# Optimization experiments

Hardware: AMD Instinct MI355X
Metric: run time of the kernel (lower is better)

## Reference

```python
import jax, jax.numpy as jnp
import numpy as np

B, N1, N2, D, H, L, ITERS = 256, 64, 64, 256, 8, 18, 200
DH = D // H
LAYER_NAMES = ['self', 'cross'] * 9
OFFSET_MULT, NORMAL_MULT = 0.5, 10.0
FLIP = np.array([1.0, -1.0, -1.0], dtype=np.float32)


def setup_inputs() -> dict:
    key = jax.random.key(0)
    ks = jax.random.split(key, 16)
    s = 0.02
    inp = {
        'planeApp1': jax.random.normal(ks[0], (B, N1, D), jnp.float32),
        'planeApp2': jax.random.normal(ks[1], (B, N2, D), jnp.float32),
        'matcher_inputCam': jax.random.normal(ks[2], (B, 7), jnp.float32),
        'parameters1_local': jax.random.normal(ks[3], (B, N1, 3), jnp.float32),
        'parameters2_local': jax.random.normal(ks[4], (B, N2, 3), jnp.float32),
        'app_W': jax.random.normal(ks[5], (D, D), jnp.float32) * s,
        'app_b': jnp.zeros((D,), jnp.float32),
        'desc_W': jax.random.normal(ks[6], (D, D), jnp.float32) * s,
        'desc_b': jnp.zeros((D,), jnp.float32),
        'bin_score': jnp.asarray(1.0, jnp.float32),
        'gnn_Wq': jax.random.normal(ks[7], (L, D, D), jnp.float32) * s,
        'gnn_Wk': jax.random.normal(ks[8], (L, D, D), jnp.float32) * s,
        'gnn_Wv': jax.random.normal(ks[9], (L, D, D), jnp.float32) * s,
        'gnn_Wm': jax.random.normal(ks[10], (L, D, D), jnp.float32) * s,
        'gnn_W1': jax.random.normal(ks[11], (L, 2 * D, 2 * D), jnp.float32) * s,
        'gnn_W2': jax.random.normal(ks[12], (L, 2 * D, D), jnp.float32) * s,
        'gnn_ln1_g': jnp.ones((L, D), jnp.float32),
        'gnn_ln1_b': jnp.zeros((L, D), jnp.float32),
        'gnn_ln2_g': jnp.ones((L, D), jnp.float32),
        'gnn_ln2_b': jnp.zeros((L, D), jnp.float32),
    }
    return inp


def _layer_norm(x, g, b):
    m = jnp.mean(x, -1, keepdims=True)
    v = jnp.var(x, -1, keepdims=True)
    return (x - m) * jax.lax.rsqrt(v + 1e-5) * g + b


def _normalize(x):
    return x / jnp.clip(jnp.linalg.norm(x, axis=-1, keepdims=True), 1e-12)


def _quat_to_rot(q):
    q = q / jnp.linalg.norm(q, axis=-1, keepdims=True)
    w, x, y, z = q[:, 0], q[:, 1], q[:, 2], q[:, 3]
    R = jnp.stack([1 - 2 * (y * y + z * z), 2 * (x * y - w * z), 2 * (x * z + w * y),
                   2 * (x * y + w * z), 1 - 2 * (x * x + z * z), 2 * (y * z - w * x),
                   2 * (x * z - w * y), 2 * (y * z + w * x), 1 - 2 * (x * x + y * y)], axis=-1)
    return R.reshape(-1, 3, 3)


def _warp(plane, quat, tran):
    # plane [B,n,3], quat [B,4], tran [B,3] -> warped plane params [B,n,3]
    R = _quat_to_rot(quat)
    end = jnp.einsum('bij,bnj->bni', R, plane * FLIP) + tran[:, None, :]
    b = end - tran[:, None, :]
    scale = jnp.sum(end * b, -1) / (jnp.linalg.norm(b, axis=-1) + 1e-5) ** 2
    return scale[..., None] * b


def _lin_attn(q, k, v):
    # LoFTR linear attention; q [B,N,H,DH], k/v [B,M,H,DH]
    Q = jax.nn.elu(q) + 1.0
    K = jax.nn.elu(k) + 1.0
    v_len = v.shape[1]
    KV = jnp.einsum('bmhd,bmhe->bhde', K, v / v_len)
    Zden = 1.0 / (jnp.einsum('bnhd,bhd->bnh', Q, K.sum(1)) + 1e-6)
    return jnp.einsum('bnhd,bhde,bnh->bnhe', Q, KV, Zden) * v_len


def _enc_layer(x, src, Wq, Wk, Wv, Wm, W1, W2, g1, be1, g2, be2):
    Bx, N, _ = x.shape
    M = src.shape[1]
    q = (x @ Wq).reshape(Bx, N, H, DH)
    k = (src @ Wk).reshape(Bx, M, H, DH)
    v = (src @ Wv).reshape(Bx, M, H, DH)
    msg = _lin_attn(q, k, v).reshape(Bx, N, D)
    msg = _layer_norm(msg @ Wm, g1, be1)
    msg = _layer_norm(jax.nn.relu(jnp.concatenate([x, msg], -1) @ W1) @ W2, g2, be2)
    return x + msg


def reference(planeApp1, planeApp2, matcher_inputCam, parameters1_local, parameters2_local,
              app_W, app_b, desc_W, desc_b, bin_score,
              gnn_Wq, gnn_Wk, gnn_Wv, gnn_Wm, gnn_W1, gnn_W2,
              gnn_ln1_g, gnn_ln1_b, gnn_ln2_g, gnn_ln2_b):
    tran, quat = matcher_inputCam[:, :3], matcher_inputCam[:, 3:]
    # --- geometric priors (detached in the original) ---
    p2w = parameters2_local * FLIP  # warp with pose_n=1, no rot/tran
    offset2 = jnp.linalg.norm(p2w, axis=-1)  # [B,N2]
    normal2 = _normalize(p2w)
    p1_r = _warp(parameters1_local, quat, tran * 0.0)
    normal1_r = _normalize(p1_r)
    normal_dist = jnp.arccos(jnp.clip(jnp.einsum('bnd,bmd->bnm', normal1_r, normal2), -1.0, 1.0)) / np.pi * 180.0
    p1_rt = _warp(parameters1_local, quat, tran)
    offset1 = jnp.linalg.norm(p1_rt, axis=-1)  # [B,N1]
    normal1_rt = _normalize(p1_rt)
    nTn_rt = jnp.einsum('bnd,bmd->bnm', normal1_rt, normal2)
    od = jnp.where(nTn_rt < 0,
                   jnp.abs(offset1[:, :, None] + offset2[:, None, :]),
                   jnp.abs(offset1[:, :, None] - offset2[:, None, :]))
    offset_dist = jax.lax.stop_gradient(jnp.clip(od, 1e-10, 5.0))
    normal_dist = jax.lax.stop_gradient(normal_dist)
    # --- appearance projection (1x1 Conv1d == per-token linear) ---
    x0 = planeApp1 @ app_W + app_b
    x1 = planeApp2 @ app_W + app_b
    for i, name in enumerate(LAYER_NAMES):
        p = (gnn_Wq[i], gnn_Wk[i], gnn_Wv[i], gnn_Wm[i], gnn_W1[i], gnn_W2[i],
             gnn_ln1_g[i], gnn_ln1_b[i], gnn_ln2_g[i], gnn_ln2_b[i])
        if name == 'self':
            x0, x1 = _enc_layer(x0, x0, *p), _enc_layer(x1, x1, *p)
        else:
            x0, x1 = _enc_layer(x0, x1, *p), _enc_layer(x1, x0, *p)
    d1 = x0 @ desc_W + desc_b
    d2 = x1 @ desc_W + desc_b
    scores = jnp.einsum('bnd,bmd->bnm', d1, d2) / jnp.sqrt(jnp.float32(D))
    scores = scores - offset_dist / OFFSET_MULT - normal_dist / NORMAL_MULT
    # --- padded optimal transport (all rows/cols valid -> no -inf masking) ---
    pc = jnp.broadcast_to(bin_score, (B, N1, 1))
    pr = jnp.broadcast_to(bin_score, (B, 1, N2 + 1))
    Z = jnp.concatenate([jnp.concatenate([scores, pc], axis=2), pr], axis=1)  # [B,N1+1,N2+1]
    norm = -jnp.log(jnp.float32(N1 + N2))
    log_mu = jnp.broadcast_to(jnp.concatenate([jnp.full((N1,), norm), (jnp.log(jnp.float32(N2)) + norm)[None]]), (B, N1 + 1))
    log_nu = jnp.broadcast_to(jnp.concatenate([jnp.full((N2,), norm), (jnp.log(jnp.float32(N1)) + norm)[None]]), (B, N2 + 1))

    def step(carry, _):
        u, v = carry
        u = log_mu - jax.nn.logsumexp(Z + v[:, None, :], axis=2)
        v = log_nu - jax.nn.logsumexp(Z + u[:, :, None], axis=1)
        return (u, v), None

    (u, v), _ = jax.lax.scan(step, (jnp.zeros_like(log_mu), jnp.zeros_like(log_nu)), None, length=ITERS)
    return Z + u[:, :, None] + v[:, None, :] - norm
```

## Files before the change

kernel.cpp:

```cpp
#include <hip/hip_runtime.h>
#include <math.h>
#include <stddef.h>
#include <stdint.h>

typedef unsigned short u16;
typedef unsigned int   u32;

static constexpr int B_   = 256;
static constexpr int N_   = 64;
static constexpr int D_   = 256;
static constexpr int L_   = 18;
static constexpr int RM   = B_ * N_;
static constexpr int RM2  = 2 * RM;
static constexpr size_t SZb = (size_t)RM2 * D_;

typedef __attribute__((ext_vector_type(8))) short bf16x8;
typedef __attribute__((ext_vector_type(4))) float f32x4;

__device__ __forceinline__ float b2f(u16 u) {
    return __uint_as_float(((u32)u) << 16);
}
__device__ __forceinline__ u16 f2b(float f) {
    u32 x = __float_as_uint(f);
    return (u16)((x + 0x7FFFu + ((x >> 16) & 1u)) >> 16);
}
__device__ __forceinline__ void gl_lds16(const void* g, void* l) {
    __builtin_amdgcn_global_load_lds(
        (const __attribute__((address_space(1))) u32*)g,
        (__attribute__((address_space(3))) u32*)l, 16, 0, 0);
}

template<int CONCAT, int RELU, int BIAS, int OUTF, int OUTB>
__global__ __launch_bounds__(256)
void mgemm(const u16* __restrict__ A1, const u16* __restrict__ A2,
           const u16* __restrict__ Bt, const float* __restrict__ bias,
           float* __restrict__ Cf, u16* __restrict__ Cb,
           int M, int K, int splitn)
{
    __shared__ u16 As[128 * 64];
    __shared__ u16 Bs[128 * 64];
    const int tid  = threadIdx.x;
    const int w    = tid >> 6;
    const int lane = tid & 63;
    const int wr   = w >> 1, wc = w & 1;
    const int row0 = blockIdx.x * 128;
    const int col0 = blockIdx.y * 128;
    const int lr   = lane & 15;
    const int lk   = (lane >> 4) * 8;
    const int srow = lane >> 3;
    const int schk = (lane & 7) * 8;

    f32x4 acc[4][4];
    #pragma unroll
    for (int m = 0; m < 4; ++m)
        #pragma unroll
        for (int n = 0; n < 4; ++n)
            acc[m][n] = (f32x4){0.f, 0.f, 0.f, 0.f};

    for (int k0 = 0; k0 < K; k0 += 64) {
        const u16* Aeff; int kloc, lda;
        if (CONCAT) {
            if (k0 < 256) { Aeff = A1; kloc = k0; } else { Aeff = A2; kloc = k0 - 256; }
            lda = 256;
        } else { Aeff = A1; kloc = k0; lda = K; }
        #pragma unroll
        for (int q = 0; q < 4; ++q) {
            const int i = w * 4 + q;
            gl_lds16(Aeff + (size_t)(row0 + i * 8 + srow) * lda + kloc + schk,
                     &As[i * 512]);
            gl_lds16(Bt + (size_t)(col0 + i * 8 + srow) * K + k0 + schk,
                     &Bs[i * 512]);
        }
        __syncthreads();
        #pragma unroll
        for (int kk = 0; kk < 2; ++kk) {
            bf16x8 af[4], bfr[4];
            #pragma unroll
            for (int m = 0; m < 4; ++m)
                af[m] = *(const bf16x8*)&As[(wr * 64 + m * 16 + lr) * 64 + kk * 32 + lk];
            #pragma unroll
            for (int n = 0; n < 4; ++n)
                bfr[n] = *(const bf16x8*)&Bs[(wc * 64 + n * 16 + lr) * 64 + kk * 32 + lk];
            #pragma unroll
            for (int m = 0; m < 4; ++m)
                #pragma unroll
                for (int n = 0; n < 4; ++n)
                    acc[m][n] = __builtin_amdgcn_mfma_f32_16x16x32_bf16(
                        af[m], bfr[n], acc[m][n], 0, 0, 0);
        }
        __syncthreads();
    }

    const size_t cbase = (size_t)(col0 / splitn) * (size_t)M * splitn;
    const int lc0 = col0 % splitn;
    #pragma unroll
    for (int m = 0; m < 4; ++m) {
        #pragma unroll
        for (int n = 0; n < 4; ++n) {
            const int gc = lc0 + wc * 64 + n * 16 + (lane & 15);
            #pragma unroll
            for (int r = 0; r < 4; ++r) {
                const int gr = row0 + wr * 64 + m * 16 + (lane >> 4) * 4 + r;
                float v = acc[m][n][r];
                if (BIAS) v += bias[gc];
                if (RELU) v = fmaxf(v, 0.f);
                const size_t idx = cbase + (size_t)gr * splitn + gc;
                if (OUTF) Cf[idx] = v;
                if (OUTB) Cb[idx] = f2b(v);
            }
        }
    }
}

template<int RES>
__global__ __launch_bounds__(256)
void mgemm_ln(const u16* __restrict__ A, const u16* __restrict__ Bt,
              const float* __restrict__ g, const float* __restrict__ beta,
              float* __restrict__ resf, u16* __restrict__ outb, int K)
{
    __shared__ u16 As[64 * 64];
    __shared__ u16 Bs[256 * 64];
    __shared__ float rs[4][64], rq[4][64];
    const int tid  = threadIdx.x;
    const int w    = tid >> 6;
    const int lane = tid & 63;
    const int row0 = blockIdx.x * 64;
    const int lr   = lane & 15;
    const int lk   = (lane >> 4) * 8;
    const int srow = lane >> 3;
    const int schk = (lane & 7) * 8;

    f32x4 acc[4][4];
    #pragma unroll
    for (int m = 0; m < 4; ++m)
        #pragma unroll
        for (int n = 0; n < 4; ++n)
            acc[m][n] = (f32x4){0.f, 0.f, 0.f, 0.f};

    for (int k0 = 0; k0 < K; k0 += 64) {
        #pragma unroll
        for (int q = 0; q < 2; ++q) {
            const int i = w * 2 + q;
            gl_lds16(A + (size_t)(row0 + i * 8 + srow) * K + k0 + schk,
                     &As[i * 512]);
        }
        #pragma unroll
        for (int q = 0; q < 8; ++q) {
            const int i = w * 8 + q;
            gl_lds16(Bt + (size_t)(i * 8 + srow) * K + k0 + schk,
                     &Bs[i * 512]);
        }
        __syncthreads();
        #pragma unroll
        for (int kk = 0; kk < 2; ++kk) {
            bf16x8 af[4], bfr[4];
            #pragma unroll
            for (int m = 0; m < 4; ++m)
                af[m] = *(const bf16x8*)&As[(m * 16 + lr) * 64 + kk * 32 + lk];
            #pragma unroll
            for (int n = 0; n < 4; ++n)
                bfr[n] = *(const bf16x8*)&Bs[(w * 64 + n * 16 + lr) * 64 + kk * 32 + lk];
            #pragma unroll
            for (int m = 0; m < 4; ++m)
                #pragma unroll
                for (int n = 0; n < 4; ++n)
                    acc[m][n] = __builtin_amdgcn_mfma_f32_16x16x32_bf16(
                        af[m], bfr[n], acc[m][n], 0, 0, 0);
        }
        __syncthreads();
    }

    #pragma unroll
    for (int m = 0; m < 4; ++m) {
        #pragma unroll
        for (int r = 0; r < 4; ++r) {
            float s  = acc[m][0][r] + acc[m][1][r] + acc[m][2][r] + acc[m][3][r];
            float s2 = acc[m][0][r]*acc[m][0][r] + acc[m][1][r]*acc[m][1][r]
                     + acc[m][2][r]*acc[m][2][r] + acc[m][3][r]*acc[m][3][r];
            #pragma unroll
            for (int o = 1; o < 16; o <<= 1) {
                s  += __shfl_xor(s,  o);
                s2 += __shfl_xor(s2, o);
            }
            if ((lane & 15) == 0) {
                const int row = m * 16 + (lane >> 4) * 4 + r;
                rs[w][row] = s; rq[w][row] = s2;
            }
        }
    }
    __syncthreads();
    if (tid < 64) {
        const float s = rs[0][tid] + rs[1][tid] + rs[2][tid] + rs[3][tid];
        const float q = rq[0][tid] + rq[1][tid] + rq[2][tid] + rq[3][tid];
        const float mean = s * (1.f / 256.f);
        const float var  = q * (1.f / 256.f) - mean * mean;
        rs[0][tid] = mean;
        rq[0][tid] = rsqrtf(var + 1e-5f);
    }
    __syncthreads();

    float gc[4], bc[4];
    #pragma unroll
    for (int n = 0; n < 4; ++n) {
        const int col = w * 64 + n * 16 + lr;
        gc[n] = g[col]; bc[n] = beta[col];
    }
    #pragma unroll
    for (int m = 0; m < 4; ++m) {
        #pragma unroll
        for (int r = 0; r < 4; ++r) {
            const int row  = m * 16 + (lane >> 4) * 4 + r;
            const float mean = rs[0][row], inv = rq[0][row];
            const int gr = row0 + row;
            #pragma unroll
            for (int n = 0; n < 4; ++n) {
                const int col = w * 64 + n * 16 + lr;
                const size_t idx = (size_t)gr * 256 + col;
                float y = (acc[m][n][r] - mean) * inv * gc[n] + bc[n];
                if (RES) {
                    const float o = resf[idx] + y;
                    resf[idx] = o;
                    outb[idx] = f2b(o);
                } else {
                    outb[idx] = f2b(y);
                }
            }
        }
    }
}

__global__ __launch_bounds__(256)
void wtrans_kernel(const float* __restrict__ W, u16* __restrict__ Wt,
                   int K, int N, size_t in_lstride, size_t out_lstride,
                   int row_off, int ldk)
{
    __shared__ float T[64][65];
    const int k0 = blockIdx.x * 64, n0 = blockIdx.y * 64, l = blockIdx.z;
    const int t = threadIdx.x;
    const int r = t >> 2, c0 = (t & 3) * 16;
    const float* src = W + (size_t)l * in_lstride;
    #pragma unroll
    for (int q = 0; q < 4; ++q) {
        float4 v = *(const float4*)&src[(size_t)(k0 + r) * N + n0 + c0 + q * 4];
        T[r][c0 + q * 4 + 0] = v.x; T[r][c0 + q * 4 + 1] = v.y;
        T[r][c0 + q * 4 + 2] = v.z; T[r][c0 + q * 4 + 3] = v.w;
    }
    __syncthreads();
    u16 tmp[16];
    #pragma unroll
    for (int i = 0; i < 16; ++i) tmp[i] = f2b(T[c0 + i][r]);
    u16* dst = Wt + (size_t)l * out_lstride + (size_t)(row_off + n0 + r) * ldk + k0 + c0;
    *(uint4*)&dst[0] = *(const uint4*)&tmp[0];
    *(uint4*)&dst[8] = *(const uint4*)&tmp[8];
}

__global__ __launch_bounds__(256)
void cvt_kernel(const float* __restrict__ src, u16* __restrict__ dst, int n4)
{
    int i = blockIdx.x * 256 + threadIdx.x;
    if (i >= n4) return;
    float4 v = *(const float4*)&src[(size_t)i * 4];
    u16 o[4] = {f2b(v.x), f2b(v.y), f2b(v.z), f2b(v.w)};
    *(uint2*)&dst[(size_t)i * 4] = *(const uint2*)&o[0];
}

__global__ __launch_bounds__(256)
void attn_kernel(const u16* __restrict__ Q, const u16* __restrict__ K,
                 const u16* __restrict__ V, u16* __restrict__ Mout, int selfl)
{
    const int bid = blockIdx.x;
    const int h = bid & 7;
    const int b = (bid >> 3) & 255;
    const int s = bid >> 11;
    const int ss = selfl ? s : (1 - s);
    const size_t qoff = ((size_t)(s  * RM) + b * N_) * D_ + h * 32;
    const size_t koff = ((size_t)(ss * RM) + b * N_) * D_ + h * 32;

    __shared__ float Ks[64][32];
    __shared__ float Vs[64][32];
    __shared__ float Qs[64][33];
    __shared__ float KV[32][32];
    __shared__ float Ksum[32];
    __shared__ float zden[64];

    const int t = threadIdx.x;
    {
        const int m = t >> 2, d0 = (t & 3) * 8;
        uint4 kq = *(const uint4*)&K[koff + (size_t)m * D_ + d0];
        uint4 vq = *(const uint4*)&V[koff + (size_t)m * D_ + d0];
        uint4 qq = *(const uint4*)&Q[qoff + (size_t)m * D_ + d0];
        const u16* kp = (const u16*)&kq;
        const u16* vp = (const u16*)&vq;
        const u16* qp = (const u16*)&qq;
        #pragma unroll
        for (int j = 0; j < 8; ++j) {
            float kx = b2f(kp[j]);
            Ks[m][d0 + j] = kx > 0.f ? kx + 1.f : __expf(kx);
            Vs[m][d0 + j] = b2f(vp[j]);
            float qx = b2f(qp[j]);
            Qs[m][d0 + j] = qx > 0.f ? qx + 1.f : __expf(qx);
        }
    }
    __syncthreads();
    if (t < 32) {
        float sacc = 0.f;
        for (int m = 0; m < 64; ++m) sacc += Ks[m][t];
        Ksum[t] = sacc;
    }
    for (int i = t; i < 32 * 32; i += 256) {
        const int d = i >> 5, e = i & 31;
        float acc = 0.f;
        for (int m = 0; m < 64; ++m) acc += Ks[m][d] * Vs[m][e];
        KV[d][e] = acc * (1.f / 64.f);
    }
    __syncthreads();
    if (t < 64) {
        float acc = 0.f;
        for (int d = 0; d < 32; ++d) acc += Qs[t][d] * Ksum[d];
        zden[t] = 1.f / (acc + 1e-6f);
    }
    __syncthreads();
    const int n = t >> 2, eg = t & 3;
    float acc[8] = {0.f,0.f,0.f,0.f,0.f,0.f,0.f,0.f};
    for (int d = 0; d < 32; ++d) {
        const float qv = Qs[n][d];
        #pragma unroll
        for (int j = 0; j < 8; ++j) acc[j] += qv * KV[d][eg * 8 + j];
    }
    const float zm = zden[n] * 64.f;
    u16 o[8];
    #pragma unroll
    for (int j = 0; j < 8; ++j) o[j] = f2b(acc[j] * zm);
    *(uint4*)&Mout[qoff + (size_t)n * D_ + eg * 8] = *(const uint4*)&o[0];
}

__global__ __launch_bounds__(64)
void geom_kernel(const float* __restrict__ cam, const float* __restrict__ p1,
                 const float* __restrict__ p2, float* __restrict__ pen)
{
    const int b = blockIdx.x;
    const int n = threadIdx.x;

    const float tx = cam[b*7+0], ty = cam[b*7+1], tz = cam[b*7+2];
    float qw = cam[b*7+3], qx = cam[b*7+4], qy = cam[b*7+5], qz = cam[b*7+6];
    const float qn = rsqrtf(qw*qw + qx*qx + qy*qy + qz*qz);
    qw *= qn; qx *= qn; qy *= qn; qz *= qn;
    const float r00 = 1.f - 2.f*(qy*qy + qz*qz), r01 = 2.f*(qx*qy - qw*qz), r02 = 2.f*(qx*qz + qw*qy);
    const float r10 = 2.f*(qx*qy + qw*qz), r11 = 1.f - 2.f*(qx*qx + qz*qz), r12 = 2.f*(qy*qz - qw*qx);
    const float r20 = 2.f*(qx*qz - qw*qy), r21 = 2.f*(qy*qz + qw*qx), r22 = 1.f - 2.f*(qx*qx + qy*qy);

    const float px =  p1[((size_t)b*64 + n)*3 + 0];
    const float py = -p1[((size_t)b*64 + n)*3 + 1];
    const float pz = -p1[((size_t)b*64 + n)*3 + 2];
    const float ex = r00*px + r01*py + r02*pz;
    const float ey = r10*px + r11*py + r12*pz;
    const float ez = r20*px + r21*py + r22*pz;
    const float el2 = ex*ex + ey*ey + ez*ez;
    const float el  = sqrtf(el2);
    float den = el + 1e-5f; den = den * den;
    const float sr  = el2 / den;
    const float prx = sr*ex, pry = sr*ey, prz = sr*ez;
    const float prl = fmaxf(sqrtf(prx*prx + pry*pry + prz*prz), 1e-12f);
    const float n1rx = prx/prl, n1ry = pry/prl, n1rz = prz/prl;
    const float dot_eb = (ex+tx)*ex + (ey+ty)*ey + (ez+tz)*ez;
    const float st  = dot_eb / den;
    const float ptx = st*ex, pty = st*ey, ptz = st*ez;
    const float o1  = sqrtf(ptx*ptx + pty*pty + ptz*ptz);
    const float ptl = fmaxf(o1, 1e-12f);
    const float n1tx = ptx/ptl, n1ty = pty/ptl, n1tz = ptz/ptl;
    const float ux =  p2[((size_t)b*64 + n)*3 + 0];
    const float uy = -p2[((size_t)b*64 + n)*3 + 1];
    const float uz = -p2[((size_t)b*64 + n)*3 + 2];
    const float o2 = sqrtf(ux*ux + uy*uy + uz*uz);
    const float ul = fmaxf(o2, 1e-12f);

    __shared__ float S[64][4];
    S[n][0] = ux/ul; S[n][1] = uy/ul; S[n][2] = uz/ul; S[n][3] = o2;
    __syncthreads();

    const float RAD2DEG = 57.295779513082323f;
    for (int m = 0; m < 64; ++m) {
        const float nx = S[m][0], ny = S[m][1], nz = S[m][2], o2m = S[m][3];
        float cosr = n1rx*nx + n1ry*ny + n1rz*nz;
        cosr = fminf(fmaxf(cosr, -1.f), 1.f);
        const float ndist = acosf(cosr) * RAD2DEG;
        const float cost = n1tx*nx + n1ty*ny + n1tz*nz;
        float od = (cost < 0.f) ? fabsf(o1 + o2m) : fabsf(o1 - o2m);
        od = fminf(fmaxf(od, 1e-10f), 5.f);
        pen[((size_t)b*64 + n)*64 + m] = od * 2.f + ndist * 0.1f;
    }
}

__global__ __launch_bounds__(256)
void zbuild_kernel(const float* __restrict__ dfeat, const float* __restrict__ pen,
                   const float* __restrict__ binp, float* __restrict__ Z)
{
    const int b = blockIdx.x;
    const float* d1 = dfeat + (size_t)(b * 64) * 256;
    const float* d2 = dfeat + (size_t)(RM + b * 64) * 256;
    __shared__ float D1[64][65], D2[64][65];
    const int tid = threadIdx.x;
    const int txx = tid & 15, tyy = tid >> 4;
    float acc[4][4] = {{0.f,0.f,0.f,0.f},{0.f,0.f,0.f,0.f},
                       {0.f,0.f,0.f,0.f},{0.f,0.f,0.f,0.f}};
    for (int c0 = 0; c0 < 256; c0 += 64) {
        __syncthreads();
        for (int i = tid; i < 64 * 64; i += 256) {
            const int r = i >> 6, c = i & 63;
            D1[r][c] = d1[(size_t)r * 256 + c0 + c];
            D2[r][c] = d2[(size_t)r * 256 + c0 + c];
        }
        __syncthreads();
        for (int c = 0; c < 64; ++c) {
            const float a0 = D1[tyy*4+0][c], a1 = D1[tyy*4+1][c];
            const float a2 = D1[tyy*4+2][c], a3 = D1[tyy*4+3][c];
            const float b0 = D2[txx*4+0][c], b1 = D2[txx*4+1][c];
            const float b2 = D2[txx*4+2][c], b3 = D2[txx*4+3][c];
            acc[0][0] += a0*b0; acc[0][1] += a0*b1; acc[0][2] += a0*b2; acc[0][3] += a0*b3;
            acc[1][0] += a1*b0; acc[1][1] += a1*b1; acc[1][2] += a1*b2; acc[1][3] += a1*b3;
            acc[2][0] += a2*b0; acc[2][1] += a2*b1; acc[2][2] += a2*b2; acc[2][3] += a2*b3;
            acc[3][0] += a3*b0; acc[3][1] += a3*b1; acc[3][2] += a3*b2; acc[3][3] += a3*b3;
        }
    }
    const float bin = *binp;
    #pragma unroll
    for (int i = 0; i < 4; ++i)
        #pragma unroll
        for (int j = 0; j < 4; ++j) {
            const int n = tyy*4 + i, m = txx*4 + j;
            Z[(size_t)b*4225 + n*65 + m] =
                acc[i][j] * (1.f/16.f) - pen[((size_t)b*64 + n)*64 + m];
        }
    if (tid < 65) Z[(size_t)b*4225 + 64*65 + tid] = bin;
    if (tid < 64) Z[(size_t)b*4225 + tid*65 + 64] = bin;
}

__global__ __launch_bounds__(576)
void sinkhorn_kernel(const float* __restrict__ Zin, float* __restrict__ out)
{
    const int b = blockIdx.x;
    __shared__ float uu[65], vv[65];
    const int t  = threadIdx.x;
    const int rr = t >> 3, l8 = t & 7;
    const int act = (rr < 65);
    const float LOG2E = 1.4426950408889634f;
    const float LN2   = 0.69314718055994531f;

    float zrow[9], zcol[9];
    #pragma unroll
    for (int p = 0; p < 9; ++p) {
        const int j = l8 + p * 8;
        const int ok = act && (j < 65);
        zrow[p] = ok ? Zin[(size_t)b * 4225 + rr * 65 + j] * LOG2E : -3.0e38f;
        zcol[p] = ok ? Zin[(size_t)b * 4225 + j * 65 + rr] * LOG2E : -3.0e38f;
    }
    if (t < 65) vv[t] = 0.f;
    __syncthreads();

    const float mu2 = (rr < 64) ? -7.0f : -1.0f;

    for (int it = 0; it < 200; ++it) {
        {
            float m = -3.0e38f, sum = 0.f, vals[9];
            #pragma unroll
            for (int p = 0; p < 9; ++p) {
                const int j = l8 + p * 8;
                vals[p] = zrow[p] + vv[j < 65 ? j : 0];
                m = fmaxf(m, vals[p]);
            }
            #pragma unroll
            for (int p = 0; p < 9; ++p) sum += exp2f(vals[p] - m);
            #pragma unroll
            for (int o = 1; o < 8; o <<= 1) {
                const float om = __shfl_xor(m, o);
                const float os = __shfl_xor(sum, o);
                const float nm = fmaxf(m, om);
                sum = sum * exp2f(m - nm) + os * exp2f(om - nm);
                m = nm;
            }
            if (act && l8 == 0) uu[rr] = mu2 - (m + log2f(sum));
        }
        __syncthreads();
        {
            float m = -3.0e38f, sum = 0.f, vals[9];
            #pragma unroll
            for (int p = 0; p < 9; ++p) {
                const int j = l8 + p * 8;
                vals[p] = zcol[p] + uu[j < 65 ? j : 0];
                m = fmaxf(m, vals[p]);
            }
            #pragma unroll
            for (int p = 0; p < 9; ++p) sum += exp2f(vals[p] - m);
            #pragma unroll
            for (int o = 1; o < 8; o <<= 1) {
                const float om = __shfl_xor(m, o);
                const float os = __shfl_xor(sum, o);
                const float nm = fmaxf(m, om);
                sum = sum * exp2f(m - nm) + os * exp2f(om - nm);
                m = nm;
            }
            if (act && l8 == 0) vv[rr] = mu2 - (m + log2f(sum));
        }
        __syncthreads();
    }
    if (act) {
        const float ur = uu[rr];
        #pragma unroll
        for (int p = 0; p < 9; ++p) {
            const int j = l8 + p * 8;
            if (j < 65)
                out[(size_t)b * 4225 + rr * 65 + j] =
                    (zrow[p] + ur + vv[j] + 7.0f) * LN2;
        }
    }
}

extern "C" void kernel_launch(void* const* d_in, const int* in_sizes, int n_in,
                              void* d_out, int out_size, void* d_ws, size_t ws_size,
                              hipStream_t stream)
{
    const float* planeApp1 = (const float*)d_in[0];
    const float* planeApp2 = (const float*)d_in[1];
    const float* cam       = (const float*)d_in[2];
    const float* p1        = (const float*)d_in[3];
    const float* p2        = (const float*)d_in[4];
    const float* app_W     = (const float*)d_in[5];
    const float* app_b     = (const float*)d_in[6];
    const float* desc_W    = (const float*)d_in[7];
    const float* desc_b    = (const float*)d_in[8];
    const float* bin_score = (const float*)d_in[9];
    const float* Wq        = (const float*)d_in[10];
    const float* Wk        = (const float*)d_in[11];
    const float* Wv        = (const float*)d_in[12];
    const float* Wm        = (const float*)d_in[13];
    const float* W1        = (const float*)d_in[14];
    const float* W2        = (const float*)d_in[15];
    const float* ln1g      = (const float*)d_in[16];
    const float* ln1b      = (const float*)d_in[17];
    const float* ln2g      = (const float*)d_in[18];
    const float* ln2b      = (const float*)d_in[19];

    const size_t wq_elems   = (size_t)L_ * 768 * 256;
    const size_t wm_elems   = (size_t)L_ * 256 * 256;
    const size_t w1_elems   = (size_t)L_ * 512 * 512;
    const size_t w2_elems   = (size_t)L_ * 256 * 512;
    const size_t need = 5 * SZb * 2 + SZb * 4 + (size_t)B_ * 4096 * 4 +
        (wq_elems + wm_elems + w1_elems + w2_elems + 2 * 65536) * 2;
    if (ws_size < need) return;

    u16* Xb = (u16*)d_ws;
    u16* Qb = Xb + SZb;
    u16* Kb = Qb + SZb;
    u16* Vb = Kb + SZb;
    u16* Tb = Vb + SZb;
    float* Xf  = (float*)(Tb + SZb);
    float* pen = Xf + SZb;
    u16* wqkv = (u16*)(pen + (size_t)B_ * 4096);
    u16* wmt  = wqkv + wq_elems;
    u16* w1t  = wmt + wm_elems;
    u16* w2t  = w1t + w1_elems;
    u16* appt = w2t + w2_elems;
    u16* dsct = appt + 65536;
    float* outp = (float*)d_out;

    wtrans_kernel<<<dim3(4, 4, L_), 256, 0, stream>>>(Wq, wqkv, 256, 256, 65536, 768*256, 0,   256);
    wtrans_kernel<<<dim3(4, 4, L_), 256, 0, stream>>>(Wk, wqkv, 256, 256, 65536, 768*256, 256, 256);
    wtrans_kernel<<<dim3(4, 4, L_), 256, 0, stream>>>(Wv, wqkv, 256, 256, 65536, 768*256, 512, 256);
    wtrans_kernel<<<dim3(4, 4, L_), 256, 0, stream>>>(Wm, wmt,  256, 256, 65536, 65536,   0,   256);
    wtrans_kernel<<<dim3(8, 8, L_), 256, 0, stream>>>(W1, w1t,  512, 512, 262144, 262144, 0,   512);
    wtrans_kernel<<<dim3(8, 4, L_), 256, 0, stream>>>(W2, w2t,  512, 256, 131072, 131072, 0,   512);
    wtrans_kernel<<<dim3(4, 4, 1),  256, 0, stream>>>(app_W,  appt, 256, 256, 65536, 65536, 0, 256);
    wtrans_kernel<<<dim3(4, 4, 1),  256, 0, stream>>>(desc_W, dsct, 256, 256, 65536, 65536, 0, 256);

    cvt_kernel<<<(RM * D_ / 4 + 255) / 256, 256, 0, stream>>>(planeApp1, Qb, RM * D_ / 4);
    cvt_kernel<<<(RM * D_ / 4 + 255) / 256, 256, 0, stream>>>(planeApp2, Qb + (size_t)RM * D_, RM * D_ / 4);

    geom_kernel<<<B_, 64, 0, stream>>>(cam, p1, p2, pen);

    mgemm<0,0,1,1,1><<<dim3(RM2/128, 2), 256, 0, stream>>>(
        Qb, nullptr, appt, app_b, Xf, Xb, RM2, 256, 256);

    for (int i = 0; i < L_; ++i) {
        const int selfl = (i % 2 == 0) ? 1 : 0;
        mgemm<0,0,0,0,1><<<dim3(RM2/128, 6), 256, 0, stream>>>(
            Xb, nullptr, wqkv + (size_t)i*768*256, nullptr, nullptr, Qb, RM2, 256, 256);
        attn_kernel<<<2 * B_ * 8, 256, 0, stream>>>(Qb, Kb, Vb, Qb, selfl);
        mgemm_ln<0><<<RM2/64, 256, 0, stream>>>(
            Qb, wmt + (size_t)i*65536, ln1g + i*256, ln1b + i*256,
            nullptr, Tb, 256);
        mgemm<1,1,0,0,1><<<dim3(RM2/128, 4), 256, 0, stream>>>(
            Xb, Tb, w1t + (size_t)i*262144, nullptr, nullptr, Qb, RM2, 512, 512);
        mgemm_ln<1><<<RM2/64, 256, 0, stream>>>(
            Qb, w2t + (size_t)i*131072, ln2g + i*256, ln2b + i*256,
            Xf, Xb, 512);
    }

    mgemm<0,0,1,1,0><<<dim3(RM2/128, 2), 256, 0, stream>>>(
        Xb, nullptr, dsct, desc_b, (float*)Qb, nullptr, RM2, 256, 256);

    zbuild_kernel<<<B_, 256, 0, stream>>>((float*)Qb, pen, bin_score, (float*)Vb);
    sinkhorn_kernel<<<B_, 576, 0, stream>>>((float*)Vb, outp);
}
```

Baseline: 3.336 ms.

## Double-buffer GEMM LDS tiles, enlarge LN-GEMM tile, simplify Sinkhorn reductions

Both GEMM kernels now prefetch the next K-slice into a second LDS buffer while the current one feeds the MFMAs, with K a compile-time constant so the loop fully unrolls. The fused GEMM+LayerNorm kernel moves to 128-row tiles on 512 threads, halving how often each block reloads the full 256-column weight slab. The Sinkhorn loop replaces its online max/sum shuffle merge with a max reduction followed by a plain sum reduction, and pads the u/v arrays so index clamping is no longer needed. The cost is more LDS per block (about 100KB for the LN kernel), which lowers occupancy.

```diff
diff --git a/kernel.cpp b/kernel.cpp
--- a/kernel.cpp
+++ b/kernel.cpp
@@ -30,15 +30,16 @@
         (__attribute__((address_space(3))) u32*)l, 16, 0, 0);
 }
 
-template<int CONCAT, int RELU, int BIAS, int OUTF, int OUTB>
+template<int K, int CONCAT, int RELU, int BIAS, int OUTF, int OUTB>
 __global__ __launch_bounds__(256)
 void mgemm(const u16* __restrict__ A1, const u16* __restrict__ A2,
            const u16* __restrict__ Bt, const float* __restrict__ bias,
            float* __restrict__ Cf, u16* __restrict__ Cb,
-           int M, int K, int splitn)
-{
-    __shared__ u16 As[128 * 64];
-    __shared__ u16 Bs[128 * 64];
+           int M, int splitn)
+{
+    constexpr int NT = K / 64;
+    __shared__ u16 As[2][128 * 64];
+    __shared__ u16 Bs[2][128 * 64];
     const int tid  = threadIdx.x;
     const int w    = tid >> 6;
     const int lane = tid & 63;
@@ -50,14 +51,8 @@
     const int srow = lane >> 3;
     const int schk = (lane & 7) * 8;
 
-    f32x4 acc[4][4];
-    #pragma unroll
-    for (int m = 0; m < 4; ++m)
-        #pragma unroll
-        for (int n = 0; n < 4; ++n)
-            acc[m][n] = (f32x4){0.f, 0.f, 0.f, 0.f};
-
-    for (int k0 = 0; k0 < K; k0 += 64) {
+    auto stage = [&](int t, int buf) {
+        const int k0 = t * 64;
         const u16* Aeff; int kloc, lda;
         if (CONCAT) {
             if (k0 < 256) { Aeff = A1; kloc = k0; } else { Aeff = A2; kloc = k0 - 256; }
@@ -67,20 +62,34 @@
         for (int q = 0; q < 4; ++q) {
             const int i = w * 4 + q;
             gl_lds16(Aeff + (size_t)(row0 + i * 8 + srow) * lda + kloc + schk,
-                     &As[i * 512]);
-            gl_lds16(Bt + (size_t)(col0 + i * 8 + srow) * K + k0 + schk,
-                     &Bs[i * 512]);
-        }
-        __syncthreads();
+                     &As[buf][i * 512]);
+            gl_lds16(Bt + (size_t)(col0 + i * 8 + srow) * K + t * 64 + schk,
+                     &Bs[buf][i * 512]);
+        }
+    };
+
+    f32x4 acc[4][4];
+    #pragma unroll
+    for (int m = 0; m < 4; ++m)
+        #pragma unroll
+        for (int n = 0; n < 4; ++n)
+            acc[m][n] = (f32x4){0.f, 0.f, 0.f, 0.f};
+
+    stage(0, 0);
+    __syncthreads();
+    #pragma unroll
+    for (int t = 0; t < NT; ++t) {
+        const int cur = t & 1;
+        if (t + 1 < NT) stage(t + 1, cur ^ 1);
         #pragma unroll
         for (int kk = 0; kk < 2; ++kk) {
             bf16x8 af[4], bfr[4];
             #pragma unroll
             for (int m = 0; m < 4; ++m)
-                af[m] = *(const bf16x8*)&As[(wr * 64 + m * 16 + lr) * 64 + kk * 32 + lk];
+                af[m] = *(const bf16x8*)&As[cur][(wr * 64 + m * 16 + lr) * 64 + kk * 32 + lk];
             #pragma unroll
             for (int n = 0; n < 4; ++n)
-                bfr[n] = *(const bf16x8*)&Bs[(wc * 64 + n * 16 + lr) * 64 + kk * 32 + lk];
+                bfr[n] = *(const bf16x8*)&Bs[cur][(wc * 64 + n * 16 + lr) * 64 + kk * 32 + lk];
             #pragma unroll
             for (int m = 0; m < 4; ++m)
                 #pragma unroll
@@ -112,24 +121,41 @@
     }
 }
 
-template<int RES>
-__global__ __launch_bounds__(256)
+template<int K, int RES>
+__global__ __launch_bounds__(512)
 void mgemm_ln(const u16* __restrict__ A, const u16* __restrict__ Bt,
               const float* __restrict__ g, const float* __restrict__ beta,
-              float* __restrict__ resf, u16* __restrict__ outb, int K)
-{
-    __shared__ u16 As[64 * 64];
-    __shared__ u16 Bs[256 * 64];
-    __shared__ float rs[4][64], rq[4][64];
+              float* __restrict__ resf, u16* __restrict__ outb)
+{
+    constexpr int NT = K / 64;
+    __shared__ u16 As[2][128 * 64];
+    __shared__ u16 Bs[2][256 * 64];
+    __shared__ float rs[4][128], rq[4][128];
     const int tid  = threadIdx.x;
     const int w    = tid >> 6;
     const int lane = tid & 63;
-    const int row0 = blockIdx.x * 64;
+    const int wr   = w >> 2, wc = w & 3;
+    const int row0 = blockIdx.x * 128;
     const int lr   = lane & 15;
     const int lk   = (lane >> 4) * 8;
     const int srow = lane >> 3;
     const int schk = (lane & 7) * 8;
 
+    auto stage = [&](int t, int buf) {
+        #pragma unroll
+        for (int q = 0; q < 2; ++q) {
+            const int i = w * 2 + q;
+            gl_lds16(A + (size_t)(row0 + i * 8 + srow) * K + t * 64 + schk,
+                     &As[buf][i * 512]);
+        }
+        #pragma unroll
+        for (int q = 0; q < 4; ++q) {
+            const int i = w * 4 + q;
+            gl_lds16(Bt + (size_t)(i * 8 + srow) * K + t * 64 + schk,
+                     &Bs[buf][i * 512]);
+        }
+    };
+
     f32x4 acc[4][4];
     #pragma unroll
     for (int m = 0; m < 4; ++m)
@@ -137,29 +163,21 @@
         for (int n = 0; n < 4; ++n)
             acc[m][n] = (f32x4){0.f, 0.f, 0.f, 0.f};
 
-    for (int k0 = 0; k0 < K; k0 += 64) {
-        #pragma unroll
-        for (int q = 0; q < 2; ++q) {
-            const int i = w * 2 + q;
-            gl_lds16(A + (size_t)(row0 + i * 8 + srow) * K + k0 + schk,
-                     &As[i * 512]);
-        }
-        #pragma unroll
-        for (int q = 0; q < 8; ++q) {
-            const int i = w * 8 + q;
-            gl_lds16(Bt + (size_t)(i * 8 + srow) * K + k0 + schk,
-                     &Bs[i * 512]);
-        }
-        __syncthreads();
+    stage(0, 0);
+    __syncthreads();
+    #pragma unroll
+    for (int t = 0; t < NT; ++t) {
+        const int cur = t & 1;
+        if (t + 1 < NT) stage(t + 1, cur ^ 1);
         #pragma unroll
         for (int kk = 0; kk < 2; ++kk) {
             bf16x8 af[4], bfr[4];
             #pragma unroll
             for (int m = 0; m < 4; ++m)
-                af[m] = *(const bf16x8*)&As[(m * 16 + lr) * 64 + kk * 32 + lk];
+                af[m] = *(const bf16x8*)&As[cur][(wr * 64 + m * 16 + lr) * 64 + kk * 32 + lk];
             #pragma unroll
             for (int n = 0; n < 4; ++n)
-                bfr[n] = *(const bf16x8*)&Bs[(w * 64 + n * 16 + lr) * 64 + kk * 32 + lk];
+                bfr[n] = *(const bf16x8*)&Bs[cur][(wc * 64 + n * 16 + lr) * 64 + kk * 32 + lk];
             #pragma unroll
             for (int m = 0; m < 4; ++m)
                 #pragma unroll
@@ -183,13 +201,13 @@
                 s2 += __shfl_xor(s2, o);
             }
             if ((lane & 15) == 0) {
-                const int row = m * 16 + (lane >> 4) * 4 + r;
-                rs[w][row] = s; rq[w][row] = s2;
+                const int row = wr * 64 + m * 16 + (lane >> 4) * 4 + r;
+                rs[wc][row] = s; rq[wc][row] = s2;
             }
         }
     }
     __syncthreads();
-    if (tid < 64) {
+    if (tid < 128) {
         const float s = rs[0][tid] + rs[1][tid] + rs[2][tid] + rs[3][tid];
         const float q = rq[0][tid] + rq[1][tid] + rq[2][tid] + rq[3][tid];
         const float mean = s * (1.f / 256.f);
@@ -202,19 +220,19 @@
     float gc[4], bc[4];
     #pragma unroll
     for (int n = 0; n < 4; ++n) {
-        const int col = w * 64 + n * 16 + lr;
+        const int col = wc * 64 + n * 16 + lr;
         gc[n] = g[col]; bc[n] = beta[col];
     }
     #pragma unroll
     for (int m = 0; m < 4; ++m) {
         #pragma unroll
         for (int r = 0; r < 4; ++r) {
-            const int row  = m * 16 + (lane >> 4) * 4 + r;
+            const int row  = wr * 64 + m * 16 + (lane >> 4) * 4 + r;
             const float mean = rs[0][row], inv = rq[0][row];
             const int gr = row0 + row;
             #pragma unroll
             for (int n = 0; n < 4; ++n) {
-                const int col = w * 64 + n * 16 + lr;
+                const int col = wc * 64 + n * 16 + lr;
                 const size_t idx = (size_t)gr * 256 + col;
                 float y = (acc[m][n][r] - mean) * inv * gc[n] + bc[n];
                 if (RES) {
@@ -439,7 +457,7 @@
 void sinkhorn_kernel(const float* __restrict__ Zin, float* __restrict__ out)
 {
     const int b = blockIdx.x;
-    __shared__ float uu[65], vv[65];
+    __shared__ float uu[72], vv[72];
     const int t  = threadIdx.x;
     const int rr = t >> 3, l8 = t & 7;
     const int act = (rr < 65);
@@ -454,51 +472,43 @@
         zrow[p] = ok ? Zin[(size_t)b * 4225 + rr * 65 + j] * LOG2E : -3.0e38f;
         zcol[p] = ok ? Zin[(size_t)b * 4225 + j * 65 + rr] * LOG2E : -3.0e38f;
     }
-    if (t < 65) vv[t] = 0.f;
+    if (t < 72) { vv[t] = 0.f; uu[t] = 0.f; }
     __syncthreads();
 
     const float mu2 = (rr < 64) ? -7.0f : -1.0f;
 
     for (int it = 0; it < 200; ++it) {
         {
-            float m = -3.0e38f, sum = 0.f, vals[9];
-            #pragma unroll
-            for (int p = 0; p < 9; ++p) {
-                const int j = l8 + p * 8;
-                vals[p] = zrow[p] + vv[j < 65 ? j : 0];
-                m = fmaxf(m, vals[p]);
-            }
+            float vals[9];
+            #pragma unroll
+            for (int p = 0; p < 9; ++p) vals[p] = zrow[p] + vv[l8 + p * 8];
+            float m = vals[0];
+            #pragma unroll
+            for (int p = 1; p < 9; ++p) m = fmaxf(m, vals[p]);
+            #pragma unroll
+            for (int o = 1; o < 8; o <<= 1) m = fmaxf(m, __shfl_xor(m, o));
+            float sum = 0.f;
             #pragma unroll
             for (int p = 0; p < 9; ++p) sum += exp2f(vals[p] - m);
             #pragma unroll
-            for (int o = 1; o < 8; o <<= 1) {
-                const float om = __shfl_xor(m, o);
-                const float os = __shfl_xor(sum, o);
-                const float nm = fmaxf(m, om);
-                sum = sum * exp2f(m - nm) + os * exp2f(om - nm);
-                m = nm;
-            }
+            for (int o = 1; o < 8; o <<= 1) sum += __shfl_xor(sum, o);
             if (act && l8 == 0) uu[rr] = mu2 - (m + log2f(sum));
         }
         __syncthreads();
         {
-            float m = -3.0e38f, sum = 0.f, vals[9];
-            #pragma unroll
-            for (int p = 0; p < 9; ++p) {
-                const int j = l8 + p * 8;
-                vals[p] = zcol[p] + uu[j < 65 ? j : 0];
-                m = fmaxf(m, vals[p]);
-            }
+            float vals[9];
+            #pragma unroll
+            for (int p = 0; p < 9; ++p) vals[p] = zcol[p] + uu[l8 + p * 8];
+            float m = vals[0];
+            #pragma unroll
+            for (int p = 1; p < 9; ++p) m = fmaxf(m, vals[p]);
+            #pragma unroll
+            for (int o = 1; o < 8; o <<= 1) m = fmaxf(m, __shfl_xor(m, o));
+            float sum = 0.f;
             #pragma unroll
             for (int p = 0; p < 9; ++p) sum += exp2f(vals[p] - m);
             #pragma unroll
-            for (int o = 1; o < 8; o <<= 1) {
-                const float om = __shfl_xor(m, o);
-                const float os = __shfl_xor(sum, o);
-                const float nm = fmaxf(m, om);
-                sum = sum * exp2f(m - nm) + os * exp2f(om - nm);
-                m = nm;
-            }
+            for (int o = 1; o < 8; o <<= 1) sum += __shfl_xor(sum, o);
             if (act && l8 == 0) vv[rr] = mu2 - (m + log2f(sum));
         }
         __syncthreads();
@@ -577,26 +587,26 @@
 
     geom_kernel<<<B_, 64, 0, stream>>>(cam, p1, p2, pen);
 
-    mgemm<0,0,1,1,1><<<dim3(RM2/128, 2), 256, 0, stream>>>(
-        Qb, nullptr, appt, app_b, Xf, Xb, RM2, 256, 256);
+    mgemm<256,0,0,1,1,1><<<dim3(RM2/128, 2), 256, 0, stream>>>(
+        Qb, nullptr, appt, app_b, Xf, Xb, RM2, 256);
 
     for (int i = 0; i < L_; ++i) {
         const int selfl = (i % 2 == 0) ? 1 : 0;
-        mgemm<0,0,0,0,1><<<dim3(RM2/128, 6), 256, 0, stream>>>(
-            Xb, nullptr, wqkv + (size_t)i*768*256, nullptr, nullptr, Qb, RM2, 256, 256);
+        mgemm<256,0,0,0,0,1><<<dim3(RM2/128, 6), 256, 0, stream>>>(
+            Xb, nullptr, wqkv + (size_t)i*768*256, nullptr, nullptr, Qb, RM2, 256);
         attn_kernel<<<2 * B_ * 8, 256, 0, stream>>>(Qb, Kb, Vb, Qb, selfl);
-        mgemm_ln<0><<<RM2/64, 256, 0, stream>>>(
+        mgemm_ln<256,0><<<RM2/128, 512, 0, stream>>>(
             Qb, wmt + (size_t)i*65536, ln1g + i*256, ln1b + i*256,
-            nullptr, Tb, 256);
-        mgemm<1,1,0,0,1><<<dim3(RM2/128, 4), 256, 0, stream>>>(
-            Xb, Tb, w1t + (size_t)i*262144, nullptr, nullptr, Qb, RM2, 512, 512);
-        mgemm_ln<1><<<RM2/64, 256, 0, stream>>>(
+            nullptr, Tb);
+        mgemm<512,1,1,0,0,1><<<dim3(RM2/128, 4), 256, 0, stream>>>(
+            Xb, Tb, w1t + (size_t)i*262144, nullptr, nullptr, Qb, RM2, 512);
+        mgemm_ln<512,1><<<RM2/128, 512, 0, stream>>>(
             Qb, w2t + (size_t)i*131072, ln2g + i*256, ln2b + i*256,
-            Xf, Xb, 512);
-    }
-
-    mgemm<0,0,1,1,0><<<dim3(RM2/128, 2), 256, 0, stream>>>(
-        Xb, nullptr, dsct, desc_b, (float*)Qb, nullptr, RM2, 256, 256);
+            Xf, Xb);
+    }
+
+    mgemm<256,0,0,1,1,0><<<dim3(RM2/128, 2), 256, 0, stream>>>(
+        Xb, nullptr, dsct, desc_b, (float*)Qb, nullptr, RM2, 256);
 
     zbuild_kernel<<<B_, 256, 0, stream>>>((float*)Qb, pen, bin_score, (float*)Vb);
     sinkhorn_kernel<<<B_, 576, 0, stream>>>((float*)Vb, outp);
```

After: 3.175 ms. 1.05x faster.
